# Kernel tuning notes

Measured on AMD Instinct MI355X. Metric: run time of the kernel, lower is better.

## Reference

```python
import jax, jax.numpy as jnp
import numpy as np

N = 32768; E = 262144; NS = 128; NV = 64; D = NS + 3 * NV  # 320
ES = 64; RH = 128; GH = 64; NT = 10
SQ3 = 3.0 ** 0.5


def _expand(s):
    # per-channel scale [E, NS+NV] -> [E, D]; each vector channel's scale replicated over its 3 components
    return jnp.concatenate([s[:, :NS], jnp.repeat(s[:, NS:], 3, axis=-1)], axis=-1)


def _norm(v):
    return jnp.sqrt(jnp.sum(v * v, axis=-1) + 1e-12)


def setup_inputs() -> dict:
    key = jax.random.key(0)
    ks = jax.random.split(key, 30)
    f = lambda i, shp: jax.random.normal(ks[i], shp, jnp.float32) * 0.1
    return dict(
        h=jax.random.normal(ks[0], (N, D), jnp.float32),
        edge_vec=jax.random.normal(ks[1], (E, 3), jnp.float32),
        edge_scalars=jax.random.normal(ks[2], (E, ES), jnp.float32),
        edge_dist=jax.random.uniform(ks[3], (E,), jnp.float32) * 5.0 + 0.5,
        src_idx=jax.random.randint(ks[4], (E,), 0, N),
        dst_idx=jax.random.randint(ks[5], (E,), 0, N),
        edge_type=jax.random.randint(ks[6], (E,), 0, NT),
        n_dst=N,
        rt_w=f(7, (ES, RH)), rt_b=f(8, (RH,)),
        rin_w=f(9, (RH, NS + NV)), rin_b=f(10, (NS + NV,)),
        rout_w=f(11, (RH, NS + NV)), rout_b=f(12, (NS + NV,)),
        tp_w00=f(13, (NS, NS)), tp_w01=f(14, (NS, NV)),
        tp_w10=f(15, (NV, NV)), tp_w11=f(16, (NV, NS)),
        act_w1=f(17, (NV, NV)), act_b1=f(18, (NV,)),
        act_w2=f(19, (NV, NV)), act_b2=jnp.full((NV,), 2.0, jnp.float32),
        gate_w1=f(20, (ES, GH)), gate_b1=f(21, (GH,)),
        gate_w2=f(22, (GH, 1 + NV)), gate_b2=f(23, (1 + NV,)),
        log_sigma=jnp.full((NT, 1), float(np.log(8.0)), jnp.float32),
        vr_w=f(24, (NV, NV)), vr_b=f(25, (NV,)),
        self_ws=f(26, (NS, NS)), self_bs=f(27, (NS,)),
        self_wv=f(28, (NV, NV)),
    )


def reference(h, edge_vec, edge_scalars, edge_dist, src_idx, dst_idx, edge_type, n_dst,
              rt_w, rt_b, rin_w, rin_b, rout_w, rout_b,
              tp_w00, tp_w01, tp_w10, tp_w11,
              act_w1, act_b1, act_w2, act_b2,
              gate_w1, gate_b1, gate_w2, gate_b2,
              log_sigma, vr_w, vr_b, self_ws, self_bs, self_wv):
    silu = jax.nn.silu
    # spherical harmonics (component norm, normalize=True): Y0 = 1, Y1 = sqrt(3) * unit(edge_vec)
    Y1 = SQ3 * edge_vec / _norm(edge_vec)[:, None]
    # radial network: input/output per-channel scales (1 + f(r))
    trunk = silu(edge_scalars @ rt_w + rt_b)
    scale_in = 1.0 + _expand(trunk @ rin_w + rin_b)
    scale_out = 1.0 + _expand(trunk @ rout_w + rout_b)
    hs = h[src_idx] * scale_in                                           # [E, D]
    x_s, x_v = hs[:, :NS], hs[:, NS:].reshape(E, NV, 3)
    # fully connected tensor product with the l<=1 SH; allowed paths:
    #   0e x 0e -> 0e, 1o x 1o -> 0e (dot / sqrt3), 0e x 1o -> 1o, 1o x 0e -> 1o
    dot = jnp.einsum('eui,ei->eu', x_v, Y1) / SQ3                        # [E, NV]
    msg_s = x_s @ tp_w00 + dot @ tp_w11                                  # [E, NS]
    msg_v = (x_s @ tp_w01)[:, :, None] * Y1[:, None, :] \
            + jnp.einsum('eui,uw->ewi', x_v, tp_w10)                     # [E, NV, 3]
    msg_s = msg_s * scale_out[:, :NS]
    msg_v = msg_v * scale_out[:, NS:].reshape(E, NV, 3)
    # gated equivariant activation: SiLU on scalars, norm-MLP sigmoid gate on vectors
    msg_s = silu(msg_s)
    g = jax.nn.sigmoid(silu(_norm(msg_v) @ act_w1 + act_b1) @ act_w2 + act_b2)
    msg_v = msg_v * g[:, :, None]
    # edge gates with learned per-edge-type distance decay
    go = silu(edge_scalars @ gate_w1 + gate_b1) @ gate_w2 + gate_b2      # [E, 1+NV]
    sigma = jnp.exp(log_sigma)[edge_type]                                # [E, 1]
    s_gate = jax.nn.sigmoid(go[:, :1]) * jnp.exp(-edge_dist[:, None] / sigma)
    seg = lambda x: jax.ops.segment_sum(x, dst_idx, num_segments=n_dst)
    # gate-normalized mean for scalar channels
    out_s = seg(s_gate * msg_s) / (seg(s_gate) + 1e-6)                   # [n_dst, NS]
    # per-channel gated aggregation for vector channels
    v_gate = jax.nn.sigmoid(go[:, 1:])                                   # [E, NV]
    agg_v = seg((msg_v * v_gate[:, :, None]).reshape(E, NV * 3)).reshape(n_dst, NV, 3)
    agg_v = agg_v / (seg(v_gate)[:, :, None] + 1e-6)
    # direction / magnitude split + per-l-group norm rescaling (single l=1 group)
    vn = _norm(agg_v)                                                    # [n_dst, NV]
    out_v = (agg_v / (vn[:, :, None] + 1e-6)) * (vn @ vr_w + vr_b)[:, :, None]
    # self-interaction residual (block-diagonal equivariant linear)
    self_s = h[:, :NS] @ self_ws + self_bs
    self_v = jnp.einsum('nui,uw->nwi', h[:, NS:].reshape(-1, NV, 3), self_wv)
    return jnp.concatenate([out_s + self_s, (out_v + self_v).reshape(n_dst, NV * 3)], axis=-1)
```

## Files before the change

kernel.cpp:

```cpp
#include <hip/hip_runtime.h>

typedef unsigned int u32;
typedef float f32x2 __attribute__((ext_vector_type(2)));
typedef float f32x4 __attribute__((ext_vector_type(4)));
typedef short s16x8 __attribute__((ext_vector_type(8)));

#define N_NODES 32768
#define N_EDGES 262144
#define PF 65

enum : int {
  OFF_RT_W   = 0,
  OFF_RT_B   = 8192,
  OFF_RIN_W  = 8320,
  OFF_RIN_B  = 32896,
  OFF_ROUT_W = 33088,
  OFF_ROUT_B = 57664,
  OFF_TP00   = 57856,
  OFF_TP01   = 74240,
  OFF_TP10   = 82432,
  OFF_TP11   = 86528,
  OFF_ACT_W1 = 94720,
  OFF_ACT_B1 = 98816,
  OFF_ACT_W2 = 98880,
  OFF_ACT_B2 = 102976,
  OFF_GATE_W1= 103040,
  OFF_GATE_B1= 107136,
  OFF_GATE_W2= 107200,
  OFF_GATE_B2= 111360,
  OFF_LSIG   = 111428,
  OFF_VR_W   = 111440,
  OFF_VR_B   = 115536,
  OFF_SELF_WS= 115600,
  OFF_SELF_BS= 131984,
  OFF_SELF_WV= 132112,
  OFF_MSBF   = 136208,
  NWF        = 148496
};
enum : int {
  ACC_S_OFF  = NWF,
  ACC_SG_OFF = ACC_S_OFF + N_NODES*128,
  ACC_VG_OFF = ACC_SG_OFF + N_NODES,
  ACC_V_OFF  = ACC_VG_OFF + N_NODES*64,
  ACC_END    = ACC_V_OFF + N_NODES*192
};

__device__ __forceinline__ float fsilu(float x){ return x/(1.f+__expf(-x)); }
__device__ __forceinline__ float fsig (float x){ return 1.f/(1.f+__expf(-x)); }
__device__ __forceinline__ f32x2 ld2(const float* p){ return *reinterpret_cast<const f32x2*>(p); }
__device__ __forceinline__ unsigned short f2bf(float f){
  u32 x = __builtin_bit_cast(u32, f);
  u32 r = x + 0x7FFFu + ((x>>16)&1u);
  return (unsigned short)(r>>16);
}

#define SQ3f     1.7320508075688772f
#define INV_SQ3f 0.5773502691896258f

__global__ void k_zero(float* __restrict__ p, int n){
  int t = blockIdx.x*256 + threadIdx.x;
  if (t < n) p[t] = 0.f;
}

struct WCopy { const float* src[24]; int n[24]; int off[24]; };

__global__ void k_copy(WCopy w, float* __restrict__ dst){
  int t = blockIdx.x*256 + threadIdx.x;
  unsigned short* ms = reinterpret_cast<unsigned short*>(dst + OFF_MSBF);
  for (int a=0;a<24;++a){
    int n = w.n[a];
    if (t < n){
      float v = w.src[a][t];
      if (a == 2){
        int k = t/192, c = t%192;
        int dc = (c < 128) ? ((c>>4)*24 + (c&15))
                           : ((((c-128)>>3)*24) + 16 + ((c-128)&7));
        dst[w.off[a] + k*192 + dc] = v;
      } else {
        dst[w.off[a]+t] = v;
      }
      if (a == 6 || a == 9){
        int k = t/128, c = t%128;
        int kg = (a==9) ? 128+k : k;
        int ct = c>>4;
        int ks = kg>>5;
        int ln = (c&15) | (((kg>>3)&3)<<4);
        int j  = kg&7;
        ms[((ct*6+ks)*64 + ln)*8 + j] = f2bf(v);
      }
      return;
    }
    t -= n;
  }
}

__launch_bounds__(512,4)
__global__ void k_edge(const float* __restrict__ h, const float* __restrict__ evec,
                       const float* __restrict__ es_g, const float* __restrict__ edist,
                       const int* __restrict__ src_idx, const int* __restrict__ dst_idx,
                       const int* __restrict__ etype, const float* __restrict__ wf,
                       float* __restrict__ acc_s, float* __restrict__ acc_sg,
                       float* __restrict__ acc_vg, float* __restrict__ acc_v)
{
  __shared__ float smf[192*PF];
  __shared__ unsigned short x_bf[64*200];
  __shared__ float s_sgate[64];
  __shared__ int   s_dst[64];

  const int tid  = threadIdx.x;
  const int lane = tid & 63;
  const int wv   = __builtin_amdgcn_readfirstlane(tid >> 6);
  const int e0   = blockIdx.x * 64;
  const int e    = e0 + lane;

  if (tid >= 64 && tid < 128) s_dst[tid-64] = dst_idx[e0 + tid-64];

  const int srcn = src_idx[e];
  const float* hrow = h + (size_t)srcn*320;
  const float4* hrow4 = reinterpret_cast<const float4*>(hrow);

  float y0,y1,y2;
  { float vx=evec[e*3], vy=evec[e*3+1], vz=evec[e*3+2];
    float rn = SQ3f * rsqrtf(vx*vx+vy*vy+vz*vz+1e-12f);
    y0=vx*rn; y1=vy*rn; y2=vz*rn; }

  for (int lin=tid; lin<1024; lin+=512){
    int row = lin>>4, c4 = lin&15;
    float4 v = reinterpret_cast<const float4*>(es_g)[(e0+row)*16 + c4];
    smf[(c4*4+0)*PF + row] = v.x;
    smf[(c4*4+1)*PF + row] = v.y;
    smf[(c4*4+2)*PF + row] = v.z;
    smf[(c4*4+3)*PF + row] = v.w;
  }
  __syncthreads();

  { f32x2 ge2[4];
    #pragma unroll
    for (int t2=0;t2<4;++t2) ge2[t2] = ld2(wf + OFF_GATE_B1 + 8*wv + 2*t2);
    #pragma unroll 2
    for (int k=0;k<64;++k){
      float a = smf[k*PF + lane];
      const float* wr = wf + OFF_GATE_W1 + k*64 + 8*wv;
      #pragma unroll
      for (int t2=0;t2<4;++t2) ge2[t2] += a*ld2(wr + 2*t2);
    }
    #pragma unroll
    for (int t=0;t<8;++t) smf[(64 + 8*wv + t)*PF + lane] = fsilu(ge2[t>>1][t&1]);
  }
  __syncthreads();

  float vga[8];
  { float g0 = wf[OFF_GATE_B2];
    #pragma unroll
    for (int t=0;t<8;++t) vga[t] = wf[OFF_GATE_B2 + 1 + 8*wv + t];
    #pragma unroll 2
    for (int k=0;k<64;++k){
      float a = smf[(64+k)*PF + lane];
      const float* wr = wf + OFF_GATE_W2 + k*65;
      g0 += a*wr[0];
      #pragma unroll
      for (int t=0;t<8;++t) vga[t] += a*wr[1 + 8*wv + t];
    }
    #pragma unroll
    for (int t=0;t<8;++t) vga[t] = fsig(vga[t]);
    if (wv == 0){
      float sigma = __expf(wf[OFF_LSIG + etype[e]]);
      s_sgate[lane] = fsig(g0) * __expf(-edist[e]/sigma);
    }
  }
  __syncthreads();

  { f32x2 acc2[8];
    #pragma unroll
    for (int j2=0;j2<8;++j2) acc2[j2] = ld2(wf + OFF_RT_B + 16*wv + 2*j2);
    #pragma unroll 2
    for (int k=0;k<64;++k){
      float a = smf[k*PF + lane];
      const float* wr = wf + OFF_RT_W + k*128 + 16*wv;
      #pragma unroll
      for (int j2=0;j2<8;++j2) acc2[j2] += a*ld2(wr + 2*j2);
    }
    #pragma unroll
    for (int j=0;j<16;++j) smf[(64 + 16*wv + j)*PF + lane] = fsilu(acc2[j>>1][j&1]);
  }
  __syncthreads();

  f32x2 sregS2[8], sregV2[4];
  #pragma unroll
  for (int i2=0;i2<8;++i2) sregS2[i2] = 1.f + ld2(wf + OFF_RIN_B + 16*wv + 2*i2);
  #pragma unroll
  for (int t2=0;t2<4;++t2) sregV2[t2] = 1.f + ld2(wf + OFF_RIN_B + 128 + 8*wv + 2*t2);
  #pragma unroll 2
  for (int k=0;k<128;++k){
    float a = smf[(64+k)*PF + lane];
    const float* wi = wf + OFF_RIN_W + k*192 + 24*wv;
    #pragma unroll
    for (int i2=0;i2<8;++i2) sregS2[i2] += a*ld2(wi + 2*i2);
    #pragma unroll
    for (int t2=0;t2<4;++t2) sregV2[t2] += a*ld2(wi + 16 + 2*t2);
  }

  f32x2 svv2[4];
  #pragma unroll
  for (int t2=0;t2<4;++t2) svv2[t2] = 0.f;

  u32* xb32 = reinterpret_cast<u32*>(x_bf);

  if (wv < 4){
    #pragma unroll
    for (int q=0;q<4;++q){
      float4 v = hrow4[4*wv + q];
      int s = 16*wv + 4*q;
      float x0 = v.x*sregS2[2*q+0][0];
      float x1 = v.y*sregS2[2*q+0][1];
      float x2 = v.z*sregS2[2*q+1][0];
      float x3 = v.w*sregS2[2*q+1][1];
      smf[(s+0)*PF + lane] = x0;
      smf[(s+1)*PF + lane] = x1;
      smf[(s+2)*PF + lane] = x2;
      smf[(s+3)*PF + lane] = x3;
      xb32[lane*100 + (s>>1)    ] = (u32)f2bf(x0) | ((u32)f2bf(x1)<<16);
      xb32[lane*100 + (s>>1) + 1] = (u32)f2bf(x2) | ((u32)f2bf(x3)<<16);
    }
  }
  __syncthreads();
  #pragma unroll 2
  for (int k=0;k<64;++k){
    float a = smf[k*PF + lane];
    const float* w1p = wf + OFF_TP01 + k*64 + 8*wv;
    #pragma unroll
    for (int t2=0;t2<4;++t2) svv2[t2] += a*ld2(w1p + 2*t2);
  }
  __syncthreads();
  if (wv >= 4){
    #pragma unroll
    for (int q=0;q<4;++q){
      float4 v = hrow4[4*wv + q];
      int gcol = 16*wv + 4*q;
      int s = gcol - 64;
      float x0 = v.x*sregS2[2*q+0][0];
      float x1 = v.y*sregS2[2*q+0][1];
      float x2 = v.z*sregS2[2*q+1][0];
      float x3 = v.w*sregS2[2*q+1][1];
      smf[(s+0)*PF + lane] = x0;
      smf[(s+1)*PF + lane] = x1;
      smf[(s+2)*PF + lane] = x2;
      smf[(s+3)*PF + lane] = x3;
      xb32[lane*100 + (gcol>>1)    ] = (u32)f2bf(x0) | ((u32)f2bf(x1)<<16);
      xb32[lane*100 + (gcol>>1) + 1] = (u32)f2bf(x2) | ((u32)f2bf(x3)<<16);
    }
  }
  __syncthreads();
  #pragma unroll 2
  for (int k=0;k<64;++k){
    float a = smf[k*PF + lane];
    const float* w1p = wf + OFF_TP01 + (64+k)*64 + 8*wv;
    #pragma unroll
    for (int t2=0;t2<4;++t2) svv2[t2] += a*ld2(w1p + 2*t2);
  }
  __syncthreads();

  f32x2 mv2[3][4];
  #pragma unroll
  for (int t2=0;t2<4;++t2){
    mv2[0][t2] = svv2[t2]*y0; mv2[1][t2] = svv2[t2]*y1; mv2[2][t2] = svv2[t2]*y2;
  }

  for (int vc=0; vc<4; ++vc){
    if ((wv>>1) == vc){
      const int half = wv & 1;
      float dreg[8];
      #pragma unroll
      for (int t=0;t<8;++t) dreg[t]=0.f;
      #pragma unroll
      for (int q=0;q<6;++q){
        float4 v = hrow4[32 + 6*wv + q];
        float vv[4] = {v.x, v.y, v.z, v.w};
        #pragma unroll
        for (int c=0;c<4;++c){
          int l = 4*q + c;
          int t = l/3, d = l - 3*t;
          float x = vv[c]*sregV2[t>>1][t&1];
          smf[(3*(8*half + t) + d)*PF + lane] = x;
          dreg[t] += x * (d==0 ? y0 : (d==1 ? y1 : y2));
        }
      }
      #pragma unroll
      for (int t=0;t<8;++t)
        x_bf[lane*200 + 128 + 16*vc + 8*half + t] = f2bf(dreg[t]*INV_SQ3f);
    }
    __syncthreads();
    #pragma unroll 2
    for (int ul=0; ul<16; ++ul){
      float x0 = smf[(3*ul+0)*PF + lane];
      float x1 = smf[(3*ul+1)*PF + lane];
      float x2 = smf[(3*ul+2)*PF + lane];
      const float* wr = wf + OFF_TP10 + (16*vc + ul)*64 + 8*wv;
      #pragma unroll
      for (int t2=0;t2<4;++t2){
        f32x2 wt2 = ld2(wr + 2*t2);
        mv2[0][t2] += x0*wt2; mv2[1][t2] += x1*wt2; mv2[2][t2] += x2*wt2;
      }
    }
    __syncthreads();
  }

  f32x2 souts2[8], soutv2[4];
  #pragma unroll
  for (int j2=0;j2<8;++j2) souts2[j2] = 1.f + ld2(wf + OFF_ROUT_B + 16*wv + 2*j2);
  #pragma unroll
  for (int t2=0;t2<4;++t2) soutv2[t2] = 1.f + ld2(wf + OFF_ROUT_B + 128 + 8*wv + 2*t2);
  #pragma unroll 2
  for (int k=0;k<128;++k){
    float a = smf[(64+k)*PF + lane];
    const float* wo = wf + OFF_ROUT_W + k*192;
    #pragma unroll
    for (int j2=0;j2<8;++j2) souts2[j2] += a*ld2(wo + 16*wv + 2*j2);
    #pragma unroll
    for (int t2=0;t2<4;++t2) soutv2[t2] += a*ld2(wo + 128 + 8*wv + 2*t2);
  }
  __syncthreads();

  { const int etile = wv & 3, g = wv >> 2;
    const int erow = (etile<<4) + (lane&15);
    const int kgrp = (lane>>4)<<3;
    const s16x8* ms8 = reinterpret_cast<const s16x8*>(wf + OFF_MSBF);
    f32x4 dacc[4];
    #pragma unroll
    for (int i=0;i<4;++i) dacc[i] = f32x4{0.f,0.f,0.f,0.f};
    #pragma unroll
    for (int ks=0;ks<6;++ks){
      s16x8 af = *reinterpret_cast<const s16x8*>(x_bf + erow*200 + ks*32 + kgrp);
      #pragma unroll
      for (int i=0;i<4;++i){
        int ct = 4*g + i;
        dacc[i] = __builtin_amdgcn_mfma_f32_16x16x32_bf16(af, ms8[(ct*6+ks)*64 + lane], dacc[i], 0,0,0);
      }
    }
    #pragma unroll
    for (int i=0;i<4;++i){
      int c = (4*g+i)*16 + (lane&15);
      #pragma unroll
      for (int r=0;r<4;++r){
        int ee = (etile<<4) + ((lane>>4)<<2) + r;
        smf[(64 + c)*PF + ee] = dacc[i][r];
      }
    }
  }
  __syncthreads();

  f32x2 msg2[8];
  #pragma unroll
  for (int j2=0;j2<8;++j2){
    msg2[j2][0] = smf[(64 + 16*wv + 2*j2+0)*PF + lane];
    msg2[j2][1] = smf[(64 + 16*wv + 2*j2+1)*PF + lane];
  }

  #pragma unroll
  for (int j2=0;j2<8;++j2){
    f32x2 m = msg2[j2]*souts2[j2];
    msg2[j2][0] = fsilu(m[0]); msg2[j2][1] = fsilu(m[1]);
  }
  #pragma unroll
  for (int t2=0;t2<4;++t2){
    mv2[0][t2] *= soutv2[t2]; mv2[1][t2] *= soutv2[t2]; mv2[2][t2] *= soutv2[t2];
  }
  #pragma unroll
  for (int t=0;t<8;++t){
    float m0 = mv2[0][t>>1][t&1], m1 = mv2[1][t>>1][t&1], m2 = mv2[2][t>>1][t&1];
    float vn = sqrtf(m0*m0 + m1*m1 + m2*m2 + 1e-12f);
    smf[(8*wv + t)*PF + lane] = vn;
  }
  __syncthreads();

  { f32x2 a12[4];
    #pragma unroll
    for (int t2=0;t2<4;++t2) a12[t2] = ld2(wf + OFF_ACT_B1 + 8*wv + 2*t2);
    #pragma unroll 2
    for (int k=0;k<64;++k){
      float a = smf[k*PF + lane];
      const float* wr = wf + OFF_ACT_W1 + k*64 + 8*wv;
      #pragma unroll
      for (int t2=0;t2<4;++t2) a12[t2] += a*ld2(wr + 2*t2);
    }
    #pragma unroll
    for (int t=0;t<8;++t) smf[(64 + 8*wv + t)*PF + lane] = fsilu(a12[t>>1][t&1]);
  }
  __syncthreads();

  { f32x2 gq2[4];
    #pragma unroll
    for (int t2=0;t2<4;++t2) gq2[t2] = ld2(wf + OFF_ACT_B2 + 8*wv + 2*t2);
    #pragma unroll 2
    for (int k=0;k<64;++k){
      float a = smf[(64+k)*PF + lane];
      const float* wr = wf + OFF_ACT_W2 + k*64 + 8*wv;
      #pragma unroll
      for (int t2=0;t2<4;++t2) gq2[t2] += a*ld2(wr + 2*t2);
    }
    #pragma unroll
    for (int t=0;t<8;++t){
      float g = fsig(gq2[t>>1][t&1]);
      mv2[0][t>>1][t&1] *= g; mv2[1][t>>1][t&1] *= g; mv2[2][t>>1][t&1] *= g;
    }
  }
  __syncthreads();

  { float sg = s_sgate[lane];
    #pragma unroll
    for (int j=0;j<16;++j) smf[(16*wv + j)*PF + lane] = sg*msg2[j>>1][j&1];
  }
  __syncthreads();
  for (int lin=tid; lin<8192; lin+=512){
    int row = lin >> 7, ch = lin & 127;
    atomicAdd(acc_s + (size_t)s_dst[row]*128 + ch, smf[ch*PF + row]);
  }
  __syncthreads();
  if (wv < 4){
    #pragma unroll
    for (int t=0;t<8;++t){
      int u = 8*wv + t;
      float vgt = vga[t];
      smf[(3*u+0)*PF + lane] = vgt*mv2[0][t>>1][t&1];
      smf[(3*u+1)*PF + lane] = vgt*mv2[1][t>>1][t&1];
      smf[(3*u+2)*PF + lane] = vgt*mv2[2][t>>1][t&1];
    }
  }
  __syncthreads();
  for (int lin=tid; lin<6144; lin+=512){
    int row = lin / 96, ch = lin % 96;
    atomicAdd(acc_v + (size_t)s_dst[row]*192 + ch, smf[ch*PF + row]);
  }
  __syncthreads();
  if (wv >= 4){
    #pragma unroll
    for (int t=0;t<8;++t){
      int um = 8*(wv-4) + t;
      float vgt = vga[t];
      smf[(3*um+0)*PF + lane] = vgt*mv2[0][t>>1][t&1];
      smf[(3*um+1)*PF + lane] = vgt*mv2[1][t>>1][t&1];
      smf[(3*um+2)*PF + lane] = vgt*mv2[2][t>>1][t&1];
    }
  }
  __syncthreads();
  for (int lin=tid; lin<6144; lin+=512){
    int row = lin / 96, ch = lin % 96;
    atomicAdd(acc_v + (size_t)s_dst[row]*192 + 96 + ch, smf[ch*PF + row]);
  }
  __syncthreads();
  #pragma unroll
  for (int t=0;t<8;++t) smf[(8*wv + t)*PF + lane] = vga[t];
  __syncthreads();
  for (int lin=tid; lin<4096; lin+=512){
    int row = lin >> 6, ch = lin & 63;
    atomicAdd(acc_vg + (size_t)s_dst[row]*64 + ch, smf[ch*PF + row]);
  }
  if (tid < 64) atomicAdd(acc_sg + s_dst[tid], s_sgate[tid]);
}

__launch_bounds__(256,2)
__global__ void k_node(const float* __restrict__ h, const float* __restrict__ wf,
                       const float* __restrict__ acc_s, const float* __restrict__ acc_sg,
                       const float* __restrict__ acc_vg, const float* __restrict__ acc_v,
                       float* __restrict__ out)
{
  __shared__ float smf[160*PF];
  const int tid  = threadIdx.x;
  const int lane = tid & 63;
  const int wv   = __builtin_amdgcn_readfirstlane(tid >> 6);
  const int n0   = blockIdx.x * 64;
  const int n    = n0 + lane;
  const int w0   = 16*wv;

  float agg[16][3], vnr[16];
  f32x2 sva2[3][8];
  #pragma unroll
  for (int t=0;t<16;++t){
    float inv = 1.f/(acc_vg[n*64 + w0 + t] + 1e-6f);
    agg[t][0] = acc_v[n*192 + (w0+t)*3 + 0]*inv;
    agg[t][1] = acc_v[n*192 + (w0+t)*3 + 1]*inv;
    agg[t][2] = acc_v[n*192 + (w0+t)*3 + 2]*inv;
    vnr[t] = sqrtf(agg[t][0]*agg[t][0]+agg[t][1]*agg[t][1]+agg[t][2]*agg[t][2]+1e-12f);
    smf[(96 + w0 + t)*PF + lane] = vnr[t];
  }
  #pragma unroll
  for (int t2=0;t2<8;++t2){ sva2[0][t2]=0.f; sva2[1][t2]=0.f; sva2[2][t2]=0.f; }

  f32x2 outs2[16];
  #pragma unroll
  for (int j2=0;j2<16;++j2) outs2[j2] = ld2(wf + OFF_SELF_BS + 32*wv + 2*j2);

  for (int cc=0; cc<2; ++cc){
    for (int lin=tid; lin<1024; lin+=256){
      int row = lin>>4, c4 = lin&15;
      float4 v = reinterpret_cast<const float4*>(h)[(n0+row)*80 + cc*16 + c4];
      smf[(c4*4+0)*PF + row] = v.x;
      smf[(c4*4+1)*PF + row] = v.y;
      smf[(c4*4+2)*PF + row] = v.z;
      smf[(c4*4+3)*PF + row] = v.w;
    }
    __syncthreads();
    #pragma unroll 2
    for (int k=0;k<64;++k){
      float a = smf[k*PF + lane];
      const float* wr = wf + OFF_SELF_WS + (cc*64+k)*128 + 32*wv;
      #pragma unroll
      for (int j2=0;j2<16;++j2) outs2[j2] += a*ld2(wr + 2*j2);
    }
    __syncthreads();
  }
  for (int cc=0; cc<2; ++cc){
    for (int lin=tid; lin<1536; lin+=256){
      int row = lin/24, c6 = lin%24;
      float4 v = reinterpret_cast<const float4*>(h)[(n0+row)*80 + 32 + cc*24 + c6];
      smf[(c6*4+0)*PF + row] = v.x;
      smf[(c6*4+1)*PF + row] = v.y;
      smf[(c6*4+2)*PF + row] = v.z;
      smf[(c6*4+3)*PF + row] = v.w;
    }
    __syncthreads();
    #pragma unroll 2
    for (int ul=0; ul<32; ++ul){
      float x0 = smf[(3*ul+0)*PF + lane];
      float x1 = smf[(3*ul+1)*PF + lane];
      float x2 = smf[(3*ul+2)*PF + lane];
      const float* wr = wf + OFF_SELF_WV + (cc*32+ul)*64 + w0;
      #pragma unroll
      for (int t2=0;t2<8;++t2){
        f32x2 wt2 = ld2(wr + 2*t2);
        sva2[0][t2] += x0*wt2; sva2[1][t2] += x1*wt2; sva2[2][t2] += x2*wt2;
      }
    }
    __syncthreads();
  }

  f32x2 rv2[8];
  #pragma unroll
  for (int t2=0;t2<8;++t2) rv2[t2] = ld2(wf + OFF_VR_B + w0 + 2*t2);
  #pragma unroll 2
  for (int k=0;k<64;++k){
    float a = smf[(96+k)*PF + lane];
    const float* wr = wf + OFF_VR_W + k*64 + w0;
    #pragma unroll
    for (int t2=0;t2<8;++t2) rv2[t2] += a*ld2(wr + 2*t2);
  }

  { float inv = 1.f/(acc_sg[n] + 1e-6f);
    const float* ap = acc_s + (size_t)n*128 + 32*wv;
    #pragma unroll
    for (int j2=0;j2<16;++j2) outs2[j2] += ld2(ap + 2*j2)*inv;
  }

  float* orow = out + (size_t)n*320;
  { float4* o4 = reinterpret_cast<float4*>(orow + 32*wv);
    #pragma unroll
    for (int j=0;j<8;++j){
      float4 v;
      v.x=outs2[2*j+0][0]; v.y=outs2[2*j+0][1];
      v.z=outs2[2*j+1][0]; v.w=outs2[2*j+1][1];
      o4[j] = v;
    }
  }
  { float vbuf[48];
    #pragma unroll
    for (int t=0;t<16;++t){
      float sc = rv2[t>>1][t&1]/(vnr[t]+1e-6f);
      vbuf[t*3+0] = agg[t][0]*sc + sva2[0][t>>1][t&1];
      vbuf[t*3+1] = agg[t][1]*sc + sva2[1][t>>1][t&1];
      vbuf[t*3+2] = agg[t][2]*sc + sva2[2][t>>1][t&1];
    }
    float4* o4 = reinterpret_cast<float4*>(orow + 128 + 48*wv);
    #pragma unroll
    for (int j=0;j<12;++j){
      float4 v; v.x=vbuf[4*j]; v.y=vbuf[4*j+1]; v.z=vbuf[4*j+2]; v.w=vbuf[4*j+3];
      o4[j] = v;
    }
  }
}

extern "C" void kernel_launch(void* const* d_in, const int* in_sizes, int n_in,
                              void* d_out, int out_size, void* d_ws, size_t ws_size,
                              hipStream_t stream) {
  const float* h     = (const float*)d_in[0];
  const float* evec  = (const float*)d_in[1];
  const float* es    = (const float*)d_in[2];
  const float* edist = (const float*)d_in[3];
  const int* srcI    = (const int*)d_in[4];
  const int* dstI    = (const int*)d_in[5];
  const int* etyp    = (const int*)d_in[6];

  float* wsf    = (float*)d_ws;
  float* acc_s  = wsf + ACC_S_OFF;
  float* acc_sg = wsf + ACC_SG_OFF;
  float* acc_vg = wsf + ACC_VG_OFF;
  float* acc_v  = wsf + ACC_V_OFF;

  WCopy wc;
  const int ns[24]  = {8192,128,24576,192,24576,192,16384,8192,4096,8192,4096,64,4096,64,
                       4096,64,4160,65,10,4096,64,16384,128,4096};
  const int offs[24]= {OFF_RT_W,OFF_RT_B,OFF_RIN_W,OFF_RIN_B,OFF_ROUT_W,OFF_ROUT_B,
                       OFF_TP00,OFF_TP01,OFF_TP10,OFF_TP11,OFF_ACT_W1,OFF_ACT_B1,
                       OFF_ACT_W2,OFF_ACT_B2,OFF_GATE_W1,OFF_GATE_B1,OFF_GATE_W2,OFF_GATE_B2,
                       OFF_LSIG,OFF_VR_W,OFF_VR_B,OFF_SELF_WS,OFF_SELF_BS,OFF_SELF_WV};
  for (int a=0;a<24;++a){ wc.src[a] = (const float*)d_in[8+a]; wc.n[a]=ns[a]; wc.off[a]=offs[a]; }
  hipLaunchKernelGGL(k_copy, dim3(533), dim3(256), 0, stream, wc, wsf);

  { int nz = ACC_END - ACC_S_OFF;
    hipLaunchKernelGGL(k_zero, dim3((nz+255)/256), dim3(256), 0, stream, acc_s, nz); }

  hipLaunchKernelGGL(k_edge, dim3(N_EDGES/64), dim3(512), 0, stream,
                     h, evec, es, edist, srcI, dstI, etyp, wsf,
                     acc_s, acc_sg, acc_vg, acc_v);
  hipLaunchKernelGGL(k_node, dim3(N_NODES/64), dim3(256), 0, stream,
                     h, wsf, acc_s, acc_sg, acc_vg, acc_v, (float*)d_out);
}
```

Baseline: 1.336 ms.

## Compute radial in/out linears with split-bf16 MFMA instead of scalar FMA

Moves the two 128x192 radial scale matmuls (rin, rout) from per-lane scalar fp32 FMA loops onto bf16 MFMA. To keep near-fp32 accuracy, it splits both the trunk activations and the weights into hi/lo bf16 parts and issues three MFMAs per step. The weights are pre-swizzled into MFMA fragment layout in the copy kernel, and results are staged through shared memory. Shared memory shrinks (smf from 192 to 128 rows, trunk buffers aliased with x_bf), which may raise occupancy, at the cost of extra barriers and some residual precision loss.

```diff
diff --git a/kernel.cpp b/kernel.cpp
--- a/kernel.cpp
+++ b/kernel.cpp
@@ -35,7 +35,11 @@
   OFF_SELF_BS= 131984,
   OFF_SELF_WV= 132112,
   OFF_MSBF   = 136208,
-  NWF        = 148496
+  OFF_RINHI  = 148496,
+  OFF_RINLO  = 160784,
+  OFF_ROUTHI = 173072,
+  OFF_ROUTLO = 185360,
+  NWF        = 197648
 };
 enum : int {
   ACC_S_OFF  = NWF,
@@ -53,6 +57,9 @@
   u32 r = x + 0x7FFFu + ((x>>16)&1u);
   return (unsigned short)(r>>16);
 }
+__device__ __forceinline__ float bf2f(unsigned short h){
+  u32 x = ((u32)h)<<16; return __builtin_bit_cast(float, x);
+}
 
 #define SQ3f     1.7320508075688772f
 #define INV_SQ3f 0.5773502691896258f
@@ -71,13 +78,23 @@
     int n = w.n[a];
     if (t < n){
       float v = w.src[a][t];
-      if (a == 2){
+      dst[w.off[a]+t] = v;
+      if (a == 2 || a == 4){
         int k = t/192, c = t%192;
-        int dc = (c < 128) ? ((c>>4)*24 + (c&15))
-                           : ((((c-128)>>3)*24) + 16 + ((c-128)&7));
-        dst[w.off[a] + k*192 + dc] = v;
-      } else {
-        dst[w.off[a]+t] = v;
+        int ct = c>>4;
+        int ks = k>>5;
+        int ln = (c&15) | (((k>>3)&3)<<4);
+        int j  = k&7;
+        int idx = ((ct*4+ks)*64 + ln)*8 + j;
+        unsigned short hi = f2bf(v);
+        unsigned short lo = f2bf(v - bf2f(hi));
+        if (a == 2){
+          reinterpret_cast<unsigned short*>(dst + OFF_RINHI)[idx] = hi;
+          reinterpret_cast<unsigned short*>(dst + OFF_RINLO)[idx] = lo;
+        } else {
+          reinterpret_cast<unsigned short*>(dst + OFF_ROUTHI)[idx] = hi;
+          reinterpret_cast<unsigned short*>(dst + OFF_ROUTLO)[idx] = lo;
+        }
       }
       if (a == 6 || a == 9){
         int k = t/128, c = t%128;
@@ -102,10 +119,14 @@
                        float* __restrict__ acc_s, float* __restrict__ acc_sg,
                        float* __restrict__ acc_vg, float* __restrict__ acc_v)
 {
-  __shared__ float smf[192*PF];
-  __shared__ unsigned short x_bf[64*200];
+  __shared__ float smf[128*PF];
+  __shared__ unsigned short tkbuf[2*64*136];
   __shared__ float s_sgate[64];
   __shared__ int   s_dst[64];
+
+  unsigned short* trunk_hi = tkbuf;
+  unsigned short* trunk_lo = tkbuf + 64*136;
+  unsigned short* x_bf     = tkbuf;
 
   const int tid  = threadIdx.x;
   const int lane = tid & 63;
@@ -180,25 +201,128 @@
       #pragma unroll
       for (int j2=0;j2<8;++j2) acc2[j2] += a*ld2(wr + 2*j2);
     }
-    #pragma unroll
-    for (int j=0;j<16;++j) smf[(64 + 16*wv + j)*PF + lane] = fsilu(acc2[j>>1][j&1]);
-  }
-  __syncthreads();
-
-  f32x2 sregS2[8], sregV2[4];
-  #pragma unroll
-  for (int i2=0;i2<8;++i2) sregS2[i2] = 1.f + ld2(wf + OFF_RIN_B + 16*wv + 2*i2);
-  #pragma unroll
-  for (int t2=0;t2<4;++t2) sregV2[t2] = 1.f + ld2(wf + OFF_RIN_B + 128 + 8*wv + 2*t2);
-  #pragma unroll 2
-  for (int k=0;k<128;++k){
-    float a = smf[(64+k)*PF + lane];
-    const float* wi = wf + OFF_RIN_W + k*192 + 24*wv;
-    #pragma unroll
-    for (int i2=0;i2<8;++i2) sregS2[i2] += a*ld2(wi + 2*i2);
-    #pragma unroll
-    for (int t2=0;t2<4;++t2) sregV2[t2] += a*ld2(wi + 16 + 2*t2);
-  }
+    u32* th32 = reinterpret_cast<u32*>(trunk_hi);
+    u32* tl32 = reinterpret_cast<u32*>(trunk_lo);
+    #pragma unroll
+    for (int j2=0;j2<8;++j2){
+      float t0 = fsilu(acc2[j2][0]), t1 = fsilu(acc2[j2][1]);
+      unsigned short h0 = f2bf(t0), h1 = f2bf(t1);
+      unsigned short l0 = f2bf(t0 - bf2f(h0)), l1 = f2bf(t1 - bf2f(h1));
+      th32[(lane*136 + 16*wv)/2 + j2] = (u32)h0 | ((u32)h1<<16);
+      tl32[(lane*136 + 16*wv)/2 + j2] = (u32)l0 | ((u32)l1<<16);
+    }
+  }
+  __syncthreads();
+
+  const int etile = wv & 3, g = wv >> 2;
+  const int erow  = etile*16 + (lane&15);
+  const int kg    = (lane>>4)<<3;
+  s16x8 ahi[4], alo[4];
+  #pragma unroll
+  for (int ks=0;ks<4;++ks){
+    ahi[ks] = *reinterpret_cast<const s16x8*>(trunk_hi + erow*136 + ks*32 + kg);
+    alo[ks] = *reinterpret_cast<const s16x8*>(trunk_lo + erow*136 + ks*32 + kg);
+  }
+
+  float sregS[16], sregV[8], souts[16], soutv[8];
+  const s16x8* rinhi8  = reinterpret_cast<const s16x8*>(wf + OFF_RINHI);
+  const s16x8* rinlo8  = reinterpret_cast<const s16x8*>(wf + OFF_RINLO);
+  const s16x8* routhi8 = reinterpret_cast<const s16x8*>(wf + OFF_ROUTHI);
+  const s16x8* routlo8 = reinterpret_cast<const s16x8*>(wf + OFF_ROUTLO);
+
+  #pragma unroll
+  for (int i=0;i<3;++i){
+    int ct = 3*g + i;
+    float bias = 1.f + wf[OFF_RIN_B + ct*16 + (lane&15)];
+    f32x4 d = {bias,bias,bias,bias};
+    #pragma unroll
+    for (int ks=0;ks<4;++ks){
+      s16x8 bh = rinhi8[(ct*4+ks)*64 + lane];
+      d = __builtin_amdgcn_mfma_f32_16x16x32_bf16(ahi[ks], bh, d, 0,0,0);
+      d = __builtin_amdgcn_mfma_f32_16x16x32_bf16(ahi[ks], rinlo8[(ct*4+ks)*64 + lane], d, 0,0,0);
+      d = __builtin_amdgcn_mfma_f32_16x16x32_bf16(alo[ks], bh, d, 0,0,0);
+    }
+    int cl = ct*16 + (lane&15);
+    #pragma unroll
+    for (int r=0;r<4;++r) smf[cl*PF + etile*16 + ((lane>>4)<<2) + r] = d[r];
+  }
+  __syncthreads();
+  if (wv < 6){
+    #pragma unroll
+    for (int i=0;i<16;++i) sregS[i] = smf[(16*wv+i)*PF + lane];
+  }
+  __syncthreads();
+  #pragma unroll
+  for (int i=0;i<3;++i){
+    int ct = 6 + 3*g + i;
+    float bias = 1.f + wf[OFF_RIN_B + ct*16 + (lane&15)];
+    f32x4 d = {bias,bias,bias,bias};
+    #pragma unroll
+    for (int ks=0;ks<4;++ks){
+      s16x8 bh = rinhi8[(ct*4+ks)*64 + lane];
+      d = __builtin_amdgcn_mfma_f32_16x16x32_bf16(ahi[ks], bh, d, 0,0,0);
+      d = __builtin_amdgcn_mfma_f32_16x16x32_bf16(ahi[ks], rinlo8[(ct*4+ks)*64 + lane], d, 0,0,0);
+      d = __builtin_amdgcn_mfma_f32_16x16x32_bf16(alo[ks], bh, d, 0,0,0);
+    }
+    int cl = ct*16 + (lane&15) - 96;
+    #pragma unroll
+    for (int r=0;r<4;++r) smf[cl*PF + etile*16 + ((lane>>4)<<2) + r] = d[r];
+  }
+  __syncthreads();
+  if (wv >= 6){
+    #pragma unroll
+    for (int i=0;i<16;++i) sregS[i] = smf[(16*wv+i-96)*PF + lane];
+  }
+  #pragma unroll
+  for (int t=0;t<8;++t) sregV[t] = smf[(32 + 8*wv + t)*PF + lane];
+  __syncthreads();
+
+  #pragma unroll
+  for (int i=0;i<3;++i){
+    int ct = 3*g + i;
+    float bias = 1.f + wf[OFF_ROUT_B + ct*16 + (lane&15)];
+    f32x4 d = {bias,bias,bias,bias};
+    #pragma unroll
+    for (int ks=0;ks<4;++ks){
+      s16x8 bh = routhi8[(ct*4+ks)*64 + lane];
+      d = __builtin_amdgcn_mfma_f32_16x16x32_bf16(ahi[ks], bh, d, 0,0,0);
+      d = __builtin_amdgcn_mfma_f32_16x16x32_bf16(ahi[ks], routlo8[(ct*4+ks)*64 + lane], d, 0,0,0);
+      d = __builtin_amdgcn_mfma_f32_16x16x32_bf16(alo[ks], bh, d, 0,0,0);
+    }
+    int cl = ct*16 + (lane&15);
+    #pragma unroll
+    for (int r=0;r<4;++r) smf[cl*PF + etile*16 + ((lane>>4)<<2) + r] = d[r];
+  }
+  __syncthreads();
+  if (wv < 6){
+    #pragma unroll
+    for (int i=0;i<16;++i) souts[i] = smf[(16*wv+i)*PF + lane];
+  }
+  __syncthreads();
+  #pragma unroll
+  for (int i=0;i<3;++i){
+    int ct = 6 + 3*g + i;
+    float bias = 1.f + wf[OFF_ROUT_B + ct*16 + (lane&15)];
+    f32x4 d = {bias,bias,bias,bias};
+    #pragma unroll
+    for (int ks=0;ks<4;++ks){
+      s16x8 bh = routhi8[(ct*4+ks)*64 + lane];
+      d = __builtin_amdgcn_mfma_f32_16x16x32_bf16(ahi[ks], bh, d, 0,0,0);
+      d = __builtin_amdgcn_mfma_f32_16x16x32_bf16(ahi[ks], routlo8[(ct*4+ks)*64 + lane], d, 0,0,0);
+      d = __builtin_amdgcn_mfma_f32_16x16x32_bf16(alo[ks], bh, d, 0,0,0);
+    }
+    int cl = ct*16 + (lane&15) - 96;
+    #pragma unroll
+    for (int r=0;r<4;++r) smf[cl*PF + etile*16 + ((lane>>4)<<2) + r] = d[r];
+  }
+  __syncthreads();
+  if (wv >= 6){
+    #pragma unroll
+    for (int i=0;i<16;++i) souts[i] = smf[(16*wv+i-96)*PF + lane];
+  }
+  #pragma unroll
+  for (int t=0;t<8;++t) soutv[t] = smf[(32 + 8*wv + t)*PF + lane];
+  __syncthreads();
 
   f32x2 svv2[4];
   #pragma unroll
@@ -211,10 +335,10 @@
     for (int q=0;q<4;++q){
       float4 v = hrow4[4*wv + q];
       int s = 16*wv + 4*q;
-      float x0 = v.x*sregS2[2*q+0][0];
-      float x1 = v.y*sregS2[2*q+0][1];
-      float x2 = v.z*sregS2[2*q+1][0];
-      float x3 = v.w*sregS2[2*q+1][1];
+      float x0 = v.x*sregS[4*q+0];
+      float x1 = v.y*sregS[4*q+1];
+      float x2 = v.z*sregS[4*q+2];
+      float x3 = v.w*sregS[4*q+3];
       smf[(s+0)*PF + lane] = x0;
       smf[(s+1)*PF + lane] = x1;
       smf[(s+2)*PF + lane] = x2;
@@ -238,10 +362,10 @@
       float4 v = hrow4[4*wv + q];
       int gcol = 16*wv + 4*q;
       int s = gcol - 64;
-      float x0 = v.x*sregS2[2*q+0][0];
-      float x1 = v.y*sregS2[2*q+0][1];
-      float x2 = v.z*sregS2[2*q+1][0];
-      float x3 = v.w*sregS2[2*q+1][1];
+      float x0 = v.x*sregS[4*q+0];
+      float x1 = v.y*sregS[4*q+1];
+      float x2 = v.z*sregS[4*q+2];
+      float x3 = v.w*sregS[4*q+3];
       smf[(s+0)*PF + lane] = x0;
       smf[(s+1)*PF + lane] = x1;
       smf[(s+2)*PF + lane] = x2;
@@ -280,7 +404,7 @@
         for (int c=0;c<4;++c){
           int l = 4*q + c;
           int t = l/3, d = l - 3*t;
-          float x = vv[c]*sregV2[t>>1][t&1];
+          float x = vv[c]*sregV[t];
           smf[(3*(8*half + t) + d)*PF + lane] = x;
           dreg[t] += x * (d==0 ? y0 : (d==1 ? y1 : y2));
         }
@@ -305,32 +429,13 @@
     __syncthreads();
   }
 
-  f32x2 souts2[8], soutv2[4];
-  #pragma unroll
-  for (int j2=0;j2<8;++j2) souts2[j2] = 1.f + ld2(wf + OFF_ROUT_B + 16*wv + 2*j2);
-  #pragma unroll
-  for (int t2=0;t2<4;++t2) soutv2[t2] = 1.f + ld2(wf + OFF_ROUT_B + 128 + 8*wv + 2*t2);
-  #pragma unroll 2
-  for (int k=0;k<128;++k){
-    float a = smf[(64+k)*PF + lane];
-    const float* wo = wf + OFF_ROUT_W + k*192;
-    #pragma unroll
-    for (int j2=0;j2<8;++j2) souts2[j2] += a*ld2(wo + 16*wv + 2*j2);
-    #pragma unroll
-    for (int t2=0;t2<4;++t2) soutv2[t2] += a*ld2(wo + 128 + 8*wv + 2*t2);
-  }
-  __syncthreads();
-
-  { const int etile = wv & 3, g = wv >> 2;
-    const int erow = (etile<<4) + (lane&15);
-    const int kgrp = (lane>>4)<<3;
-    const s16x8* ms8 = reinterpret_cast<const s16x8*>(wf + OFF_MSBF);
+  { const s16x8* ms8 = reinterpret_cast<const s16x8*>(wf + OFF_MSBF);
     f32x4 dacc[4];
     #pragma unroll
     for (int i=0;i<4;++i) dacc[i] = f32x4{0.f,0.f,0.f,0.f};
     #pragma unroll
     for (int ks=0;ks<6;++ks){
-      s16x8 af = *reinterpret_cast<const s16x8*>(x_bf + erow*200 + ks*32 + kgrp);
+      s16x8 af = *reinterpret_cast<const s16x8*>(x_bf + erow*200 + ks*32 + kg);
       #pragma unroll
       for (int i=0;i<4;++i){
         int ct = 4*g + i;
@@ -341,10 +446,8 @@
     for (int i=0;i<4;++i){
       int c = (4*g+i)*16 + (lane&15);
       #pragma unroll
-      for (int r=0;r<4;++r){
-        int ee = (etile<<4) + ((lane>>4)<<2) + r;
-        smf[(64 + c)*PF + ee] = dacc[i][r];
-      }
+      for (int r=0;r<4;++r)
+        smf[c*PF + etile*16 + ((lane>>4)<<2) + r] = dacc[i][r];
     }
   }
   __syncthreads();
@@ -352,18 +455,19 @@
   f32x2 msg2[8];
   #pragma unroll
   for (int j2=0;j2<8;++j2){
-    msg2[j2][0] = smf[(64 + 16*wv + 2*j2+0)*PF + lane];
-    msg2[j2][1] = smf[(64 + 16*wv + 2*j2+1)*PF + lane];
-  }
-
-  #pragma unroll
-  for (int j2=0;j2<8;++j2){
-    f32x2 m = msg2[j2]*souts2[j2];
-    msg2[j2][0] = fsilu(m[0]); msg2[j2][1] = fsilu(m[1]);
-  }
-  #pragma unroll
-  for (int t2=0;t2<4;++t2){
-    mv2[0][t2] *= soutv2[t2]; mv2[1][t2] *= soutv2[t2]; mv2[2][t2] *= soutv2[t2];
+    msg2[j2][0] = smf[(16*wv + 2*j2+0)*PF + lane];
+    msg2[j2][1] = smf[(16*wv + 2*j2+1)*PF + lane];
+  }
+  __syncthreads();
+
+  #pragma unroll
+  for (int j=0;j<16;++j){
+    float m = msg2[j>>1][j&1]*souts[j];
+    msg2[j>>1][j&1] = fsilu(m);
+  }
+  #pragma unroll
+  for (int t=0;t<8;++t){
+    mv2[0][t>>1][t&1] *= soutv[t]; mv2[1][t>>1][t&1] *= soutv[t]; mv2[2][t>>1][t&1] *= soutv[t];
   }
   #pragma unroll
   for (int t=0;t<8;++t){
@@ -400,8 +504,8 @@
     }
     #pragma unroll
     for (int t=0;t<8;++t){
-      float g = fsig(gq2[t>>1][t&1]);
-      mv2[0][t>>1][t&1] *= g; mv2[1][t>>1][t&1] *= g; mv2[2][t>>1][t&1] *= g;
+      float gg = fsig(gq2[t>>1][t&1]);
+      mv2[0][t>>1][t&1] *= gg; mv2[1][t>>1][t&1] *= gg; mv2[2][t>>1][t&1] *= gg;
     }
   }
   __syncthreads();
```

After: 1.279 ms. 1.04x faster.
